# Kernel optimization log

Measured on AMD Instinct MI355X. Metric: run time of the kernel, lower is better.

Reference implementation:

```python
import jax, jax.numpy as jnp
import numpy as np

BS, L, H, D = 4, 1024, 12, 768   # docs, seq len, attn heads, hidden
NE, M, P = 42, 96, 42 * 42        # max entities (min_height), mentions/doc, ht pairs
OFFSET = 1                        # bert/roberta [CLS] offset


def setup_inputs() -> dict:
    key = jax.random.key(0)
    k1, k2, k3, k4, k5 = jax.random.split(key, 5)
    sequence_output = jax.random.normal(k1, (BS, L, D), jnp.float32)
    attention = jax.random.uniform(k2, (BS, H, L, L), jnp.float32)
    mention_pos = jax.random.randint(k3, (BS, M), 0, L - OFFSET - 1).astype(jnp.int32)
    mention_entity = jnp.sort(jax.random.randint(k4, (BS, M), 0, NE), axis=-1).astype(jnp.int32)
    hts = jax.random.randint(k5, (BS, P, 2), 0, NE).astype(jnp.int32)
    return {"sequence_output": sequence_output, "attention": attention,
            "mention_pos": mention_pos, "mention_entity": mention_entity, "hts": hts}


def _per_doc_entities(seq, att, pos, ent):
    # seq [L,D], att [H,L,L], pos [M] mention token idx, ent [M] entity segment id
    idx = pos + OFFSET
    m_emb = seq[idx]                              # [M,D]  gathered mention embeddings
    m_att = jnp.transpose(att[:, idx], (1, 0, 2))  # [M,H,L] gathered mention attentions
    counts = jax.ops.segment_sum(jnp.ones((M,), seq.dtype), ent, num_segments=NE)
    has = counts > 0
    # mean-pool attentions per entity (zeros for empty entities, as in torch code)
    e_att = jax.ops.segment_sum(m_att, ent, num_segments=NE) / jnp.maximum(counts, 1.0)[:, None, None]
    # stable logsumexp-pool embeddings per entity
    seg_max = jax.ops.segment_max(m_emb, ent, num_segments=NE)      # -inf for empty segments
    seg_max = jnp.where(has[:, None], seg_max, 0.0)
    seg_sum = jax.ops.segment_sum(jnp.exp(m_emb - seg_max[ent]), ent, num_segments=NE)
    e_emb = jnp.where(has[:, None], jnp.log(jnp.maximum(seg_sum, 1e-30)) + seg_max, 0.0)
    return e_emb, e_att                           # [NE,D], [NE,H,L]


def _channel_map(seq, e_att):
    # all-pairs (h_att * t_att).mean(heads), normalize over tokens, contract with seq
    pair = jnp.einsum('ahl,bhl->abl', e_att, e_att) / H      # [NE,NE,L]
    pair = pair / (pair.sum(-1, keepdims=True) + 1e-5)
    return jnp.einsum('abl,ld->abd', pair, seq)              # [NE,NE,D]


def reference(sequence_output, attention, mention_pos, mention_entity, hts):
    e_emb, e_att = jax.vmap(_per_doc_entities)(sequence_output, attention,
                                               mention_pos, mention_entity)
    hss = jax.vmap(lambda emb, ht: emb[ht[:, 0]])(e_emb, hts).reshape(BS * P, D)
    tss = jax.vmap(lambda emb, ht: emb[ht[:, 1]])(e_emb, hts).reshape(BS * P, D)
    feature_map = jax.vmap(_channel_map)(sequence_output, e_att)  # [BS,NE,NE,D]
    return hss, tss, feature_map
```

## Files before the change

kernel.cpp:

```cpp
#include <hip/hip_runtime.h>
#include <hip/hip_bf16.h>

#define BSZ   4
#define LSEQ  1024
#define NH    12
#define DDIM  768
#define NEN   42
#define NM    96
#define NPAIR (NEN*NEN)
#define OFF   1

typedef short bf16x8 __attribute__((ext_vector_type(8)));
typedef float f32x4  __attribute__((ext_vector_type(4)));

__device__ __forceinline__ float bf2f(unsigned short u) {
    union { unsigned u; float f; } c; c.u = ((unsigned)u) << 16; return c.f;
}

typedef const __attribute__((address_space(1))) unsigned int glb_u32;
typedef __attribute__((address_space(3))) unsigned int lds_u32;
__device__ __forceinline__ void glds16(const void* g, void* l) {
    __builtin_amdgcn_global_load_lds((glb_u32*)g, (lds_u32*)l, 16, 0, 0);
}

#define NLC   2
#define EMB_CNT  (BSZ*NEN*DDIM)
#define PSUM_CNT (BSZ*NLC*NPAIR)
#define EATT_CNT (BSZ*NEN*NH*LSEQ)
#define PTIL_BYTES ((size_t)BSZ*NPAIR*LSEQ)

#define ATT_TOTAL (BSZ*NEN*NH)

#define TEN   6
#define NTILE 7
#define NTRIT (NTILE*(NTILE+1)/2)
#define LCHK  512
#define PAIR_BLKS (NTRIT*NLC*BSZ)
#define T_BLKS    ((LSEQ/32)*(DDIM/32)*BSZ)
#define EMB_BLKS  (BSZ*NEN*3)
#define MID2_TOTAL (PAIR_BLKS + T_BLKS + EMB_BLKS)

#define BM 128
#define BN 64
#define BK 128
#define MT 14
#define NT (DDIM/BN)
#define FMAP_BLKS (MT*NT*BSZ)
#define GATH_BLKS (BSZ*NPAIR/4)
#define TAIL_TOTAL (FMAP_BLKS + GATH_BLKS)

__global__ __launch_bounds__(256) void att_kernel(
        const float* __restrict__ att,
        const int* __restrict__ mpos,
        const int* __restrict__ ment,
        __hip_bfloat16* __restrict__ e_att) {
    __shared__ int sp[NM];
    __shared__ int se[NM];
    __shared__ int list[NM];
    __shared__ int pcnt;
    int id = blockIdx.x;
    int h = id % NH;
    int e = (id / NH) % NEN;
    int b = id / (NH * NEN);
    int t = threadIdx.x;
    if (t < NM) { sp[t] = mpos[b*NM + t] + OFF; se[t] = ment[b*NM + t]; }
    __syncthreads();
    if (t == 0) {
        int c = 0;
        for (int m = 0; m < NM; ++m) if (se[m] == e) list[c++] = sp[m];
        pcnt = c;
    }
    __syncthreads();
    int cnt = pcnt;
    const float* ab = att + ((size_t)(b*NH + h)) * LSEQ * LSEQ;
    float4 acc = {0.f, 0.f, 0.f, 0.f};
    for (int m = 0; m < cnt; ++m) {
        float4 v = ((const float4*)(ab + (size_t)list[m]*LSEQ))[t];
        acc.x += v.x; acc.y += v.y; acc.z += v.z; acc.w += v.w;
    }
    float inv = cnt ? 1.f / (float)cnt : 0.f;
    union { ushort4 u4; __hip_bfloat16 hh[4]; } pk;
    pk.hh[0] = __float2bfloat16(acc.x * inv);
    pk.hh[1] = __float2bfloat16(acc.y * inv);
    pk.hh[2] = __float2bfloat16(acc.z * inv);
    pk.hh[3] = __float2bfloat16(acc.w * inv);
    ((ushort4*)(e_att + ((size_t)(b*NEN + e)*NH + h)*LSEQ))[t] = pk.u4;
}

__global__ __launch_bounds__(256) void mid2_kernel(
        const float* __restrict__ seq,
        const __hip_bfloat16* __restrict__ e_att,
        const int* __restrict__ mpos,
        const int* __restrict__ ment,
        unsigned char* __restrict__ ptil,
        float* __restrict__ psum,
        unsigned char* __restrict__ seqT,
        float* __restrict__ e_emb) {
    __shared__ __align__(16) char smraw[4352];
    const int bid = blockIdx.x;
    const int t = threadIdx.x;

    if (bid < PAIR_BLKS) {
        int tri = bid % NTRIT;
        int lc  = (bid / NTRIT) % NLC;
        int b   = bid / (NTRIT * NLC);
        int ta = 0, rem = tri;
        while (rem >= NTILE - ta) { rem -= NTILE - ta; ++ta; }
        int tb = ta + rem;
        int l = lc * LCHK + t * 2;

        const __hip_bfloat16* ebase = e_att + (size_t)b*NEN*NH*LSEQ + l;
        float sx[TEN][TEN], sy[TEN][TEN];
        #pragma unroll
        for (int i = 0; i < TEN; ++i)
            #pragma unroll
            for (int j = 0; j < TEN; ++j) { sx[i][j] = 0.f; sy[i][j] = 0.f; }

        #pragma unroll 4
        for (int h = 0; h < NH; ++h) {
            float xax[TEN], xay[TEN], xbx[TEN], xby[TEN];
            #pragma unroll
            for (int e = 0; e < TEN; ++e) {
                ushort2 u = *(const ushort2*)(ebase + ((size_t)(ta*TEN+e)*NH + h)*LSEQ);
                xax[e] = bf2f(u.x); xay[e] = bf2f(u.y);
            }
            #pragma unroll
            for (int e = 0; e < TEN; ++e) {
                ushort2 u = *(const ushort2*)(ebase + ((size_t)(tb*TEN+e)*NH + h)*LSEQ);
                xbx[e] = bf2f(u.x); xby[e] = bf2f(u.y);
            }
            #pragma unroll
            for (int i = 0; i < TEN; ++i)
                #pragma unroll
                for (int j = 0; j < TEN; ++j) {
                    sx[i][j] += xax[i] * xbx[j];
                    sy[i][j] += xay[i] * xby[j];
                }
        }

        unsigned char* pbase = ptil + (size_t)b*NPAIR*LSEQ + l;
        #pragma unroll
        for (int i = 0; i < TEN; ++i) {
            #pragma unroll
            for (int j = 0; j < TEN; ++j) {
                int w = __builtin_amdgcn_cvt_pk_fp8_f32(sx[i][j], sy[i][j], 0, false);
                unsigned short q = (unsigned short)(w & 0xFFFF);
                int pa = ta*TEN + i, pb = tb*TEN + j;
                *(unsigned short*)(pbase + (size_t)(pa*NEN + pb)*LSEQ) = q;
                if (ta != tb)
                    *(unsigned short*)(pbase + (size_t)(pb*NEN + pa)*LSEQ) = q;
            }
        }

        int lane = t & 63, w = t >> 6;
        float (*redp)[TEN*TEN] = (float(*)[TEN*TEN])smraw;
        float keep = 0.f;
        #pragma unroll
        for (int i = 0; i < TEN; ++i) {
            #pragma unroll
            for (int j = 0; j < TEN; ++j) {
                float v = sx[i][j] + sy[i][j];
                v += __shfl_xor(v,  1, 64);
                v += __shfl_xor(v,  2, 64);
                v += __shfl_xor(v,  4, 64);
                v += __shfl_xor(v,  8, 64);
                v += __shfl_xor(v, 16, 64);
                v += __shfl_xor(v, 32, 64);
                if (lane == i*TEN + j) keep = v;
            }
        }
        if (lane < TEN*TEN) redp[w][lane] = keep;
        __syncthreads();
        if (t < TEN*TEN) {
            float v = redp[0][t] + redp[1][t] + redp[2][t] + redp[3][t];
            int i = t / TEN, j = t % TEN;
            int pa = ta*TEN + i, pb = tb*TEN + j;
            float* ps = psum + ((size_t)(b*NLC + lc))*NPAIR;
            ps[pa*NEN + pb] = v;
            if (ta != tb) ps[pb*NEN + pa] = v;
        }
    } else if (bid < PAIR_BLKS + T_BLKS) {
        int id = bid - PAIR_BLKS;
        int l0 = (id % (LSEQ/32)) * 32;
        int d0 = ((id / (LSEQ/32)) % (DDIM/32)) * 32;
        int b  = id / ((LSEQ/32) * (DDIM/32));
        float (*tile)[33] = (float(*)[33])smraw;
        int l = t >> 3, dq = (t & 7) * 4;
        float4 v = *(const float4*)(seq + ((size_t)b*LSEQ + l0 + l)*DDIM + d0 + dq);
        tile[l][dq+0] = v.x; tile[l][dq+1] = v.y;
        tile[l][dq+2] = v.z; tile[l][dq+3] = v.w;
        __syncthreads();
        int d = t >> 3, lq = (t & 7) * 4;
        int w = __builtin_amdgcn_cvt_pk_fp8_f32(tile[lq+0][d], tile[lq+1][d], 0, false);
        w     = __builtin_amdgcn_cvt_pk_fp8_f32(tile[lq+2][d], tile[lq+3][d], w, true);
        *(int*)(seqT + ((size_t)b*DDIM + d0 + d)*LSEQ + l0 + lq) = w;
    } else {
        int id = bid - PAIR_BLKS - T_BLKS;
        int chunk = id % 3;
        int e = (id / 3) % NEN;
        int b = id / (3 * NEN);
        int* sp   = (int*)smraw;
        int* se   = sp + NM;
        int* list = se + NM;
        int* pcnt = list + NM;
        if (t < NM) { sp[t] = mpos[b*NM + t] + OFF; se[t] = ment[b*NM + t]; }
        __syncthreads();
        if (t == 0) {
            int c = 0;
            for (int m = 0; m < NM; ++m) if (se[m] == e) list[c++] = sp[m];
            pcnt[0] = c;
        }
        __syncthreads();
        int cnt = pcnt[0];
        int d = chunk * 256 + t;
        const float* sq = seq + (size_t)b * LSEQ * DDIM + d;
        float mx = -1e30f;
        for (int m = 0; m < cnt; ++m) mx = fmaxf(mx, sq[(size_t)list[m] * DDIM]);
        float out = 0.f;
        if (cnt) {
            float s = 0.f;
            for (int m = 0; m < cnt; ++m) s += expf(sq[(size_t)list[m] * DDIM] - mx);
            out = logf(fmaxf(s, 1e-30f)) + mx;
        }
        e_emb[((size_t)b*NEN + e)*DDIM + d] = out;
    }
}

__global__ __launch_bounds__(256) void tail_kernel(
        const unsigned char* __restrict__ ptil,
        const unsigned char* __restrict__ seqT,
        const float* __restrict__ psum,
        const float* __restrict__ e_emb,
        const int* __restrict__ hts,
        float* __restrict__ out_h,
        float* __restrict__ out_t,
        float* __restrict__ fmap) {
    __shared__ unsigned char As[2][BM*BK];
    __shared__ unsigned char Bs[2][BN*BK];
    const int bid = blockIdx.x;
    const int t = threadIdx.x;

    if (bid >= FMAP_BLKS) {
        int id4  = bid - FMAP_BLKS;
        int grp  = t >> 6;
        int lane = t & 63;
        int id   = id4 * 4 + grp;
        int b    = id / NPAIR;
        int hi = hts[id*2 + 0];
        int ti = hts[id*2 + 1];
        const float4* eh = (const float4*)(e_emb + ((size_t)(b*NEN + hi))*DDIM);
        const float4* et = (const float4*)(e_emb + ((size_t)(b*NEN + ti))*DDIM);
        float4* oh = (float4*)(out_h + (size_t)id*DDIM);
        float4* ot = (float4*)(out_t + (size_t)id*DDIM);
        #pragma unroll
        for (int i = 0; i < 3; ++i) {
            oh[lane + 64*i] = eh[lane + 64*i];
            ot[lane + 64*i] = et[lane + 64*i];
        }
        return;
    }

    int tile = (bid & 7) * (FMAP_BLKS/8) + (bid >> 3);
    const int lane = t & 63;
    const int wid  = t >> 6;
    const int wr   = wid >> 1;
    const int wc   = wid & 1;
    const int bx = tile % MT, by = (tile / MT) % NT, b = tile / (MT*NT);
    const int r0 = bx * BM, c0 = by * BN;

    const unsigned char* Ab  = ptil + (size_t)b * NPAIR * LSEQ;
    const unsigned char* Btb = seqT + (size_t)b * DDIM * LSEQ;
    unsigned char* AsB = (unsigned char*)As;
    unsigned char* BsB = (unsigned char*)Bs;

    const f32x4 zero = {0.f, 0.f, 0.f, 0.f};
    f32x4 acc[4][2];
    #pragma unroll
    for (int m = 0; m < 4; ++m)
        #pragma unroll
        for (int n = 0; n < 2; ++n) acc[m][n] = zero;

    const int fr = lane & 15, kg = lane >> 4;

#define STAGE(buf, k0)                                                        \
    {                                                                         \
        _Pragma("unroll")                                                     \
        for (int i = 0; i < 4; ++i) {                                         \
            int L = t*16 + i*4096;                                            \
            int r = L >> 7, beta = L & 127;                                   \
            glds16(Ab + (size_t)(r0 + r)*LSEQ + (k0)                          \
                      + (beta ^ ((r & 7) << 4)),                              \
                   AsB + (buf)*16384 + L);                                    \
        }                                                                     \
        _Pragma("unroll")                                                     \
        for (int i = 0; i < 2; ++i) {                                         \
            int L = t*16 + i*4096;                                            \
            int c = L >> 7, beta = L & 127;                                   \
            glds16(Btb + (size_t)(c0 + c)*LSEQ + (k0)                         \
                      + (beta ^ ((c & 7) << 4)),                              \
                   BsB + (buf)*8192 + L);                                     \
        }                                                                     \
    }

    STAGE(0, 0);
    __syncthreads();

    int cur = 0;
    for (int ki = 0; ki < LSEQ/BK; ++ki) {
        if (ki + 1 < LSEQ/BK) STAGE(cur ^ 1, (ki + 1) * BK);

        const unsigned char* Ac = AsB + cur*16384;
        const unsigned char* Bc = BsB + cur*8192;

        #pragma unroll
        for (int ks = 0; ks < 4; ++ks) {
            long af[4], bfv[2];
            #pragma unroll
            for (int m = 0; m < 4; ++m) {
                int R = wr*64 + m*16 + fr;
                int e0 = (ks*32 + kg*8) ^ ((R & 7) << 4);
                af[m] = *(const long*)(Ac + R*128 + e0);
            }
            #pragma unroll
            for (int n = 0; n < 2; ++n) {
                int C = wc*32 + n*16 + fr;
                int e0 = (ks*32 + kg*8) ^ ((C & 7) << 4);
                bfv[n] = *(const long*)(Bc + C*128 + e0);
            }
            #pragma unroll
            for (int m = 0; m < 4; ++m)
                #pragma unroll
                for (int n = 0; n < 2; ++n)
                    acc[m][n] = __builtin_amdgcn_mfma_f32_16x16x32_fp8_fp8(
                                    af[m], bfv[n], acc[m][n], 0, 0, 0);
        }
        __syncthreads();
        cur ^= 1;
    }

    const float* psb = psum + (size_t)b * NLC * NPAIR;
    #pragma unroll
    for (int m = 0; m < 4; ++m) {
        int lr0 = wr*64 + m*16 + kg*4;
        #pragma unroll
        for (int i = 0; i < 4; ++i) {
            int row = r0 + lr0 + i;
            if (row < NPAIR) {
                float S = psb[row] + psb[NPAIR + row];
                float sc = 1.f / (S + (float)NH * 1e-5f);
                #pragma unroll
                for (int n = 0; n < 2; ++n) {
                    int col = c0 + wc*32 + n*16 + fr;
                    fmap[((size_t)b*NPAIR + row)*DDIM + col] = acc[m][n][i] * sc;
                }
            }
        }
    }
#undef STAGE
}

extern "C" void kernel_launch(void* const* d_in, const int* in_sizes, int n_in,
                              void* d_out, int out_size, void* d_ws, size_t ws_size,
                              hipStream_t stream) {
    const float* seq  = (const float*)d_in[0];
    const float* att  = (const float*)d_in[1];
    const int*   mpos = (const int*)d_in[2];
    const int*   ment = (const int*)d_in[3];
    const int*   hts  = (const int*)d_in[4];

    float* ws_f  = (float*)d_ws;
    float* e_emb = ws_f;
    float* psum  = ws_f + EMB_CNT;
    __hip_bfloat16* e_att = (__hip_bfloat16*)(ws_f + EMB_CNT + PSUM_CNT);
    unsigned char* ptil = (unsigned char*)(e_att + EATT_CNT);
    unsigned char* seqT = ptil + PTIL_BYTES;

    float* out_h = (float*)d_out;
    float* out_t = out_h + (size_t)BSZ*NPAIR*DDIM;
    float* fmap  = out_t + (size_t)BSZ*NPAIR*DDIM;

    hipLaunchKernelGGL(att_kernel, dim3(ATT_TOTAL), dim3(256), 0, stream,
                       att, mpos, ment, e_att);
    hipLaunchKernelGGL(mid2_kernel, dim3(MID2_TOTAL), dim3(256), 0, stream,
                       seq, e_att, mpos, ment, ptil, psum, seqT, e_emb);
    hipLaunchKernelGGL(tail_kernel, dim3(TAIL_TOTAL), dim3(256), 0, stream,
                       ptil, seqT, psum, e_emb, hts, out_h, out_t, fmap);
}
```

Before: 52.49 us.

## Regroup block roles across three kernels to rebalance stage dependencies

Moves the seq transpose and entity-embedding logsumexp blocks into the first kernel alongside the attention pooling, moves the hts gather blocks into the middle kernel alongside the pair-product work, and leaves the GEMM as its own kernel. Independent work now runs earlier, so the GEMM kernel no longer carries gather blocks and its large shared-memory footprint no longer applies to them. The gather blocks also run on small-LDS blocks. This may leave some stages imbalanced and shifts where the critical path sits.

Result: slower. 56.87 us (+8.3%).

```diff
diff --git a/kernel.cpp b/kernel.cpp
--- a/kernel.cpp
+++ b/kernel.cpp
@@ -29,16 +29,18 @@
 #define EATT_CNT (BSZ*NEN*NH*LSEQ)
 #define PTIL_BYTES ((size_t)BSZ*NPAIR*LSEQ)
 
-#define ATT_TOTAL (BSZ*NEN*NH)
+#define ATT_BLKS  (BSZ*NEN*NH)
+#define T_BLKS    ((LSEQ/32)*(DDIM/32)*BSZ)
+#define EMB_BLKS  (BSZ*NEN*3)
+#define K1_TOTAL  (ATT_BLKS + T_BLKS + EMB_BLKS)
 
 #define TEN   6
 #define NTILE 7
 #define NTRIT (NTILE*(NTILE+1)/2)
 #define LCHK  512
 #define PAIR_BLKS (NTRIT*NLC*BSZ)
-#define T_BLKS    ((LSEQ/32)*(DDIM/32)*BSZ)
-#define EMB_BLKS  (BSZ*NEN*3)
-#define MID2_TOTAL (PAIR_BLKS + T_BLKS + EMB_BLKS)
+#define GATH_BLKS (BSZ*NPAIR/4)
+#define K2_TOTAL  (PAIR_BLKS + GATH_BLKS)
 
 #define BM 128
 #define BN 64
@@ -46,141 +48,52 @@
 #define MT 14
 #define NT (DDIM/BN)
 #define FMAP_BLKS (MT*NT*BSZ)
-#define GATH_BLKS (BSZ*NPAIR/4)
-#define TAIL_TOTAL (FMAP_BLKS + GATH_BLKS)
-
-__global__ __launch_bounds__(256) void att_kernel(
+
+__global__ __launch_bounds__(256) void prep_kernel(
+        const float* __restrict__ seq,
         const float* __restrict__ att,
         const int* __restrict__ mpos,
         const int* __restrict__ ment,
-        __hip_bfloat16* __restrict__ e_att) {
-    __shared__ int sp[NM];
-    __shared__ int se[NM];
-    __shared__ int list[NM];
-    __shared__ int pcnt;
-    int id = blockIdx.x;
-    int h = id % NH;
-    int e = (id / NH) % NEN;
-    int b = id / (NH * NEN);
-    int t = threadIdx.x;
-    if (t < NM) { sp[t] = mpos[b*NM + t] + OFF; se[t] = ment[b*NM + t]; }
-    __syncthreads();
-    if (t == 0) {
-        int c = 0;
-        for (int m = 0; m < NM; ++m) if (se[m] == e) list[c++] = sp[m];
-        pcnt = c;
-    }
-    __syncthreads();
-    int cnt = pcnt;
-    const float* ab = att + ((size_t)(b*NH + h)) * LSEQ * LSEQ;
-    float4 acc = {0.f, 0.f, 0.f, 0.f};
-    for (int m = 0; m < cnt; ++m) {
-        float4 v = ((const float4*)(ab + (size_t)list[m]*LSEQ))[t];
-        acc.x += v.x; acc.y += v.y; acc.z += v.z; acc.w += v.w;
-    }
-    float inv = cnt ? 1.f / (float)cnt : 0.f;
-    union { ushort4 u4; __hip_bfloat16 hh[4]; } pk;
-    pk.hh[0] = __float2bfloat16(acc.x * inv);
-    pk.hh[1] = __float2bfloat16(acc.y * inv);
-    pk.hh[2] = __float2bfloat16(acc.z * inv);
-    pk.hh[3] = __float2bfloat16(acc.w * inv);
-    ((ushort4*)(e_att + ((size_t)(b*NEN + e)*NH + h)*LSEQ))[t] = pk.u4;
-}
-
-__global__ __launch_bounds__(256) void mid2_kernel(
-        const float* __restrict__ seq,
-        const __hip_bfloat16* __restrict__ e_att,
-        const int* __restrict__ mpos,
-        const int* __restrict__ ment,
-        unsigned char* __restrict__ ptil,
-        float* __restrict__ psum,
+        __hip_bfloat16* __restrict__ e_att,
         unsigned char* __restrict__ seqT,
         float* __restrict__ e_emb) {
     __shared__ __align__(16) char smraw[4352];
     const int bid = blockIdx.x;
     const int t = threadIdx.x;
 
-    if (bid < PAIR_BLKS) {
-        int tri = bid % NTRIT;
-        int lc  = (bid / NTRIT) % NLC;
-        int b   = bid / (NTRIT * NLC);
-        int ta = 0, rem = tri;
-        while (rem >= NTILE - ta) { rem -= NTILE - ta; ++ta; }
-        int tb = ta + rem;
-        int l = lc * LCHK + t * 2;
-
-        const __hip_bfloat16* ebase = e_att + (size_t)b*NEN*NH*LSEQ + l;
-        float sx[TEN][TEN], sy[TEN][TEN];
-        #pragma unroll
-        for (int i = 0; i < TEN; ++i)
-            #pragma unroll
-            for (int j = 0; j < TEN; ++j) { sx[i][j] = 0.f; sy[i][j] = 0.f; }
-
-        #pragma unroll 4
-        for (int h = 0; h < NH; ++h) {
-            float xax[TEN], xay[TEN], xbx[TEN], xby[TEN];
-            #pragma unroll
-            for (int e = 0; e < TEN; ++e) {
-                ushort2 u = *(const ushort2*)(ebase + ((size_t)(ta*TEN+e)*NH + h)*LSEQ);
-                xax[e] = bf2f(u.x); xay[e] = bf2f(u.y);
-            }
-            #pragma unroll
-            for (int e = 0; e < TEN; ++e) {
-                ushort2 u = *(const ushort2*)(ebase + ((size_t)(tb*TEN+e)*NH + h)*LSEQ);
-                xbx[e] = bf2f(u.x); xby[e] = bf2f(u.y);
-            }
-            #pragma unroll
-            for (int i = 0; i < TEN; ++i)
-                #pragma unroll
-                for (int j = 0; j < TEN; ++j) {
-                    sx[i][j] += xax[i] * xbx[j];
-                    sy[i][j] += xay[i] * xby[j];
-                }
-        }
-
-        unsigned char* pbase = ptil + (size_t)b*NPAIR*LSEQ + l;
-        #pragma unroll
-        for (int i = 0; i < TEN; ++i) {
-            #pragma unroll
-            for (int j = 0; j < TEN; ++j) {
-                int w = __builtin_amdgcn_cvt_pk_fp8_f32(sx[i][j], sy[i][j], 0, false);
-                unsigned short q = (unsigned short)(w & 0xFFFF);
-                int pa = ta*TEN + i, pb = tb*TEN + j;
-                *(unsigned short*)(pbase + (size_t)(pa*NEN + pb)*LSEQ) = q;
-                if (ta != tb)
-                    *(unsigned short*)(pbase + (size_t)(pb*NEN + pa)*LSEQ) = q;
-            }
-        }
-
-        int lane = t & 63, w = t >> 6;
-        float (*redp)[TEN*TEN] = (float(*)[TEN*TEN])smraw;
-        float keep = 0.f;
-        #pragma unroll
-        for (int i = 0; i < TEN; ++i) {
-            #pragma unroll
-            for (int j = 0; j < TEN; ++j) {
-                float v = sx[i][j] + sy[i][j];
-                v += __shfl_xor(v,  1, 64);
-                v += __shfl_xor(v,  2, 64);
-                v += __shfl_xor(v,  4, 64);
-                v += __shfl_xor(v,  8, 64);
-                v += __shfl_xor(v, 16, 64);
-                v += __shfl_xor(v, 32, 64);
-                if (lane == i*TEN + j) keep = v;
-            }
-        }
-        if (lane < TEN*TEN) redp[w][lane] = keep;
-        __syncthreads();
-        if (t < TEN*TEN) {
-            float v = redp[0][t] + redp[1][t] + redp[2][t] + redp[3][t];
-            int i = t / TEN, j = t % TEN;
-            int pa = ta*TEN + i, pb = tb*TEN + j;
-            float* ps = psum + ((size_t)(b*NLC + lc))*NPAIR;
-            ps[pa*NEN + pb] = v;
-            if (ta != tb) ps[pb*NEN + pa] = v;
-        }
-    } else if (bid < PAIR_BLKS + T_BLKS) {
-        int id = bid - PAIR_BLKS;
+    if (bid < ATT_BLKS) {
+        int id = bid;
+        int h = id % NH;
+        int e = (id / NH) % NEN;
+        int b = id / (NH * NEN);
+        int* sp   = (int*)smraw;
+        int* se   = sp + NM;
+        int* list = se + NM;
+        int* pcnt = list + NM;
+        if (t < NM) { sp[t] = mpos[b*NM + t] + OFF; se[t] = ment[b*NM + t]; }
+        __syncthreads();
+        if (t == 0) {
+            int c = 0;
+            for (int m = 0; m < NM; ++m) if (se[m] == e) list[c++] = sp[m];
+            pcnt[0] = c;
+        }
+        __syncthreads();
+        int cnt = pcnt[0];
+        const float* ab = att + ((size_t)(b*NH + h)) * LSEQ * LSEQ;
+        float4 acc = {0.f, 0.f, 0.f, 0.f};
+        for (int m = 0; m < cnt; ++m) {
+            float4 v = ((const float4*)(ab + (size_t)list[m]*LSEQ))[t];
+            acc.x += v.x; acc.y += v.y; acc.z += v.z; acc.w += v.w;
+        }
+        float inv = cnt ? 1.f / (float)cnt : 0.f;
+        union { ushort4 u4; __hip_bfloat16 hh[4]; } pk;
+        pk.hh[0] = __float2bfloat16(acc.x * inv);
+        pk.hh[1] = __float2bfloat16(acc.y * inv);
+        pk.hh[2] = __float2bfloat16(acc.z * inv);
+        pk.hh[3] = __float2bfloat16(acc.w * inv);
+        ((ushort4*)(e_att + ((size_t)(b*NEN + e)*NH + h)*LSEQ))[t] = pk.u4;
+    } else if (bid < ATT_BLKS + T_BLKS) {
+        int id = bid - ATT_BLKS;
         int l0 = (id % (LSEQ/32)) * 32;
         int d0 = ((id / (LSEQ/32)) % (DDIM/32)) * 32;
         int b  = id / ((LSEQ/32) * (DDIM/32));
@@ -195,7 +108,7 @@
         w     = __builtin_amdgcn_cvt_pk_fp8_f32(tile[lq+2][d], tile[lq+3][d], w, true);
         *(int*)(seqT + ((size_t)b*DDIM + d0 + d)*LSEQ + l0 + lq) = w;
     } else {
-        int id = bid - PAIR_BLKS - T_BLKS;
+        int id = bid - ATT_BLKS - T_BLKS;
         int chunk = id % 3;
         int e = (id / 3) % NEN;
         int b = id / (3 * NEN);
@@ -226,22 +139,99 @@
     }
 }
 
-__global__ __launch_bounds__(256) void tail_kernel(
-        const unsigned char* __restrict__ ptil,
-        const unsigned char* __restrict__ seqT,
-        const float* __restrict__ psum,
+__global__ __launch_bounds__(256) void mid_kernel(
+        const __hip_bfloat16* __restrict__ e_att,
         const float* __restrict__ e_emb,
         const int* __restrict__ hts,
+        unsigned char* __restrict__ ptil,
+        float* __restrict__ psum,
         float* __restrict__ out_h,
-        float* __restrict__ out_t,
-        float* __restrict__ fmap) {
-    __shared__ unsigned char As[2][BM*BK];
-    __shared__ unsigned char Bs[2][BN*BK];
+        float* __restrict__ out_t) {
+    __shared__ __align__(16) char smraw[640];
     const int bid = blockIdx.x;
     const int t = threadIdx.x;
 
-    if (bid >= FMAP_BLKS) {
-        int id4  = bid - FMAP_BLKS;
+    if (bid < PAIR_BLKS) {
+        int tri = bid % NTRIT;
+        int lc  = (bid / NTRIT) % NLC;
+        int b   = bid / (NTRIT * NLC);
+        int ta = 0, rem = tri;
+        while (rem >= NTILE - ta) { rem -= NTILE - ta; ++ta; }
+        int tb = ta + rem;
+        int l = lc * LCHK + t * 2;
+
+        const __hip_bfloat16* ebase = e_att + (size_t)b*NEN*NH*LSEQ + l;
+        float sx[TEN][TEN], sy[TEN][TEN];
+        #pragma unroll
+        for (int i = 0; i < TEN; ++i)
+            #pragma unroll
+            for (int j = 0; j < TEN; ++j) { sx[i][j] = 0.f; sy[i][j] = 0.f; }
+
+        #pragma unroll 4
+        for (int h = 0; h < NH; ++h) {
+            float xax[TEN], xay[TEN], xbx[TEN], xby[TEN];
+            #pragma unroll
+            for (int e = 0; e < TEN; ++e) {
+                ushort2 u = *(const ushort2*)(ebase + ((size_t)(ta*TEN+e)*NH + h)*LSEQ);
+                xax[e] = bf2f(u.x); xay[e] = bf2f(u.y);
+            }
+            #pragma unroll
+            for (int e = 0; e < TEN; ++e) {
+                ushort2 u = *(const ushort2*)(ebase + ((size_t)(tb*TEN+e)*NH + h)*LSEQ);
+                xbx[e] = bf2f(u.x); xby[e] = bf2f(u.y);
+            }
+            #pragma unroll
+            for (int i = 0; i < TEN; ++i)
+                #pragma unroll
+                for (int j = 0; j < TEN; ++j) {
+                    sx[i][j] += xax[i] * xbx[j];
+                    sy[i][j] += xay[i] * xby[j];
+                }
+        }
+
+        unsigned char* pbase = ptil + (size_t)b*NPAIR*LSEQ + l;
+        #pragma unroll
+        for (int i = 0; i < TEN; ++i) {
+            #pragma unroll
+            for (int j = 0; j < TEN; ++j) {
+                int w = __builtin_amdgcn_cvt_pk_fp8_f32(sx[i][j], sy[i][j], 0, false);
+                unsigned short q = (unsigned short)(w & 0xFFFF);
+                int pa = ta*TEN + i, pb = tb*TEN + j;
+                *(unsigned short*)(pbase + (size_t)(pa*NEN + pb)*LSEQ) = q;
+                if (ta != tb)
+                    *(unsigned short*)(pbase + (size_t)(pb*NEN + pa)*LSEQ) = q;
+            }
+        }
+
+        int lane = t & 63, w = t >> 6;
+        float (*redp)[TEN*TEN] = (float(*)[TEN*TEN])smraw;
+        float keep = 0.f;
+        #pragma unroll
+        for (int i = 0; i < TEN; ++i) {
+            #pragma unroll
+            for (int j = 0; j < TEN; ++j) {
+                float v = sx[i][j] + sy[i][j];
+                v += __shfl_xor(v,  1, 64);
+                v += __shfl_xor(v,  2, 64);
+                v += __shfl_xor(v,  4, 64);
+                v += __shfl_xor(v,  8, 64);
+                v += __shfl_xor(v, 16, 64);
+                v += __shfl_xor(v, 32, 64);
+                if (lane == i*TEN + j) keep = v;
+            }
+        }
+        if (lane < TEN*TEN) redp[w][lane] = keep;
+        __syncthreads();
+        if (t < TEN*TEN) {
+            float v = redp[0][t] + redp[1][t] + redp[2][t] + redp[3][t];
+            int i = t / TEN, j = t % TEN;
+            int pa = ta*TEN + i, pb = tb*TEN + j;
+            float* ps = psum + ((size_t)(b*NLC + lc))*NPAIR;
+            ps[pa*NEN + pb] = v;
+            if (ta != tb) ps[pb*NEN + pa] = v;
+        }
+    } else {
+        int id4  = bid - PAIR_BLKS;
         int grp  = t >> 6;
         int lane = t & 63;
         int id   = id4 * 4 + grp;
@@ -257,8 +247,18 @@
             oh[lane + 64*i] = eh[lane + 64*i];
             ot[lane + 64*i] = et[lane + 64*i];
         }
-        return;
-    }
+    }
+}
+
+__global__ __launch_bounds__(256) void gemm_kernel(
+        const unsigned char* __restrict__ ptil,
+        const unsigned char* __restrict__ seqT,
+        const float* __restrict__ psum,
+        float* __restrict__ fmap) {
+    __shared__ unsigned char As[2][BM*BK];
+    __shared__ unsigned char Bs[2][BN*BK];
+    const int bid = blockIdx.x;
+    const int t = threadIdx.x;
 
     int tile = (bid & 7) * (FMAP_BLKS/8) + (bid >> 3);
     const int lane = t & 63;
@@ -379,10 +379,10 @@
     float* out_t = out_h + (size_t)BSZ*NPAIR*DDIM;
     float* fmap  = out_t + (size_t)BSZ*NPAIR*DDIM;
 
-    hipLaunchKernelGGL(att_kernel, dim3(ATT_TOTAL), dim3(256), 0, stream,
-                       att, mpos, ment, e_att);
-    hipLaunchKernelGGL(mid2_kernel, dim3(MID2_TOTAL), dim3(256), 0, stream,
-                       seq, e_att, mpos, ment, ptil, psum, seqT, e_emb);
-    hipLaunchKernelGGL(tail_kernel, dim3(TAIL_TOTAL), dim3(256), 0, stream,
-                       ptil, seqT, psum, e_emb, hts, out_h, out_t, fmap);
-}
+    hipLaunchKernelGGL(prep_kernel, dim3(K1_TOTAL), dim3(256), 0, stream,
+                       seq, att, mpos, ment, e_att, seqT, e_emb);
+    hipLaunchKernelGGL(mid_kernel, dim3(K2_TOTAL), dim3(256), 0, stream,
+                       e_att, e_emb, hts, ptil, psum, out_h, out_t);
+    hipLaunchKernelGGL(gemm_kernel, dim3(FMAP_BLKS), dim3(256), 0, stream,
+                       ptil, seqT, psum, fmap);
+}
```
